# Kernel tuning notes

Measured on AMD Instinct MI355X. Metric: run time of the kernel, lower is better.

The kernel has to match this reference:

```python
import jax, jax.numpy as jnp
import numpy as np

EPS = 1e-8

def setup_inputs() -> dict:
    key = jax.random.key(0)
    k1, k2 = jax.random.split(key)
    B, IN, OUT, G = 32768, 256, 256, 5
    x = jax.random.normal(k1, (B, IN), dtype=jnp.float32)
    grid = jnp.linspace(-1.0, 1.0, G).astype(jnp.float32)
    coef = jax.random.normal(k2, (OUT, IN, G), dtype=jnp.float32) * 0.1
    scale = jnp.ones((OUT, IN), dtype=jnp.float32)
    bias = jnp.zeros((OUT,), dtype=jnp.float32)
    return {"x": x, "grid": grid, "coef": coef, "scale": scale, "bias": bias}

def reference(x, grid, coef, scale, bias):
    # global min-max normalization to [-1, 1]
    xmin, xmax = x.min(), x.max()
    xn = 2.0 * (x - xmin) / (xmax - xmin + EPS) - 1.0
    # cubic bump B-spline-like basis: (batch, in, grid)
    dist = jnp.abs(xn[..., None] - grid)
    basis = jnp.where(dist < 1.0, 1.0 - dist ** 3, 0.0)
    basis = basis / (basis.sum(axis=-1, keepdims=True) + EPS)
    # fused contraction over (in, grid); equals ((basis*coef).sum(-1)*scale).sum(-1)
    w = coef * scale[..., None]          # (out, in, grid)
    out = jnp.einsum('big,oig->bo', basis, w) + bias
    return out
```

## Files before the change

### kernel.cpp

```cpp
#include <hip/hip_runtime.h>
#include <stdint.h>


#define B_SZ   32768
#define IN_SZ  256
#define OUT_SZ 256
#define EPSF   1e-8f
#define NMB    2048

typedef __bf16 bf16x8 __attribute__((ext_vector_type(8)));
typedef unsigned short ushort8 __attribute__((ext_vector_type(8)));
typedef float floatx4 __attribute__((ext_vector_type(4)));

union frag_u { uint4 u; bf16x8 v; };

__device__ __forceinline__ unsigned short f2bf(float f) {
  unsigned u = __float_as_uint(f);
  u += 0x7FFFu + ((u >> 16) & 1u);
  return (unsigned short)(u >> 16);
}


__global__ void __launch_bounds__(256) prep_kernel(const float* __restrict__ coef,
                                                   const float* __restrict__ scale,
                                                   const float* __restrict__ x,
                                                   unsigned short* __restrict__ wf,
                                                   float* __restrict__ part, int n4) {
  const int t = threadIdx.x;
  if (blockIdx.x < 256) {
    int idx = blockIdx.x * 256 + t;
    int o = idx >> 8, i = idx & 255;
    float s = scale[idx];
    const float* c = coef + (size_t)idx * 5;
    ushort8 v;
    v[0] = f2bf(c[0] * s); v[1] = f2bf(c[1] * s); v[2] = f2bf(c[2] * s);
    v[3] = f2bf(c[3] * s); v[4] = f2bf(c[4] * s);
    v[5] = 0; v[6] = 0; v[7] = 0;
    int cb = o >> 4, om = o & 15;
    *(ushort8*)(wf + ((size_t)((cb * 256 + i) * 16 + om)) * 8) = v;
  } else {
    int mb = blockIdx.x - 256;
    const float4* x4 = (const float4*)x;
    int i = mb * 256 + t;
    float lmin = 1e30f, lmax = -1e30f;
    #pragma unroll
    for (int k = 0; k < 4; ++k) {
      float4 v = x4[i + k * (NMB * 256)];
      lmin = fminf(lmin, fminf(fminf(v.x, v.y), fminf(v.z, v.w)));
      lmax = fmaxf(lmax, fmaxf(fmaxf(v.x, v.y), fmaxf(v.z, v.w)));
    }
    #pragma unroll
    for (int off = 32; off >= 1; off >>= 1) {
      lmin = fminf(lmin, __shfl_down(lmin, off, 64));
      lmax = fmaxf(lmax, __shfl_down(lmax, off, 64));
    }
    __shared__ float smn[4], smx[4];
    if ((t & 63) == 0) { smn[t >> 6] = lmin; smx[t >> 6] = lmax; }
    __syncthreads();
    if (t == 0) {
      part[2 * mb]     = fminf(fminf(smn[0], smn[1]), fminf(smn[2], smn[3]));
      part[2 * mb + 1] = fmaxf(fmaxf(smx[0], smx[1]), fmaxf(smx[2], smx[3]));
    }
  }
}

__device__ __forceinline__ bf16x8 basisfrag(float xval, float scA, float scB) {
  float xn = fmaf(xval, scA, scB);
  float d0 = xn + 1.0f, d1 = xn + 0.5f, d3 = xn - 0.5f, d4 = xn - 1.0f;
  float b0 = fmaxf(fmaf(d0 * d0, -fabsf(d0), 1.0f), 0.0f);
  float b1 = fmaxf(fmaf(d1 * d1, -fabsf(d1), 1.0f), 0.0f);
  float b2 = fmaxf(fmaf(xn * xn, -fabsf(xn), 1.0f), 0.0f);
  float b3 = fmaxf(fmaf(d3 * d3, -fabsf(d3), 1.0f), 0.0f);
  float b4 = fmaxf(fmaf(d4 * d4, -fabsf(d4), 1.0f), 0.0f);
  float sum = ((b0 + b1) + (b2 + b3)) + b4;
  float inv = __builtin_amdgcn_rcpf(sum);
  b0 *= inv; b1 *= inv; b2 *= inv; b3 *= inv; b4 *= inv;
  frag_u r;
  r.u.x = __builtin_amdgcn_perm(__float_as_uint(b1), __float_as_uint(b0), 0x07060302u);
  r.u.y = __builtin_amdgcn_perm(__float_as_uint(b3), __float_as_uint(b2), 0x07060302u);
  r.u.z = __float_as_uint(b4) >> 16;
  r.u.w = 0u;
  return r.v;
}

__global__ void __launch_bounds__(256, 4) kan_gemm(
    const float* __restrict__ x,
    const unsigned short* __restrict__ wf,
    const float* __restrict__ bias,
    const float* __restrict__ part,
    float* __restrict__ out)
{
  __shared__ __align__(16) unsigned short Bb[2][8192];
  __shared__ float2 red[4];

  const int t = threadIdx.x;
  const int lane = t & 63;
  const int wm = t >> 6;
  const int l15 = lane & 15, koff = lane >> 4;
  const int bRow = blockIdx.x * 64;
  const int bCol = blockIdx.y * 128;
  const int row = bRow + wm * 16 + l15;

  auto stage = [&](int c, int buf) {
    #pragma unroll
    for (int r = 0; r < 4; ++r) {
      int s = r * 4 + wm;
      int cb = blockIdx.y * 8 + (s & 7);
      int i0 = c * 8 + (s >> 3) * 4;
      const unsigned short* src = wf + ((size_t)(cb * 256 + i0) * 16) * 8
                                     + (size_t)lane * 8;
      __builtin_amdgcn_global_load_lds(
          (const __attribute__((address_space(1))) unsigned int*)src,
          (__attribute__((address_space(3))) unsigned int*)(&Bb[buf][s * 512 + lane * 8]),
          16, 0, 0);
    }
  };

  const float* xrow = x + (size_t)row * IN_SZ;

  float xc0 = xrow[koff];
  float xc1 = xrow[4 + koff];
  stage(0, 0);

  float mn = 1e30f, mx = -1e30f;
  const float2* part2 = (const float2*)part;
  #pragma unroll
  for (int k = 0; k < NMB / 256; ++k) {
    float2 p = part2[k * 256 + t];
    mn = fminf(mn, p.x); mx = fmaxf(mx, p.y);
  }
  #pragma unroll
  for (int off = 32; off >= 1; off >>= 1) {
    mn = fminf(mn, __shfl_down(mn, off, 64));
    mx = fmaxf(mx, __shfl_down(mx, off, 64));
  }
  if (lane == 0) red[wm] = make_float2(mn, mx);
  __syncthreads();
  mn = fminf(fminf(red[0].x, red[1].x), fminf(red[2].x, red[3].x));
  mx = fmaxf(fmaxf(red[0].y, red[1].y), fmaxf(red[2].y, red[3].y));
  const float scA = 2.0f / (mx - mn + EPSF);
  const float scB = -mn * scA - 1.0f;

  floatx4 acc[8] = {};
  bf16x8 bf[8];

  auto ldsB = [&](int ktr, int buf) {
    #pragma unroll
    for (int q = 0; q < 8; ++q)
      bf[q] = *(const bf16x8*)(&Bb[buf][(ktr * 8 + q) * 512 + lane * 8]);
  };

  for (int c = 0; c < 32; ++c) {
    const int buf = c & 1;
    float xn0, xn1;

    if (c < 31) {
      xn0 = xrow[(c + 1) * 8 + koff];
      xn1 = xrow[(c + 1) * 8 + 4 + koff];
      stage(c + 1, buf ^ 1);
    }
    __builtin_amdgcn_sched_barrier(0);
    if (c < 31) asm volatile("s_waitcnt vmcnt(6)");
    else        asm volatile("s_waitcnt vmcnt(0)");
    __builtin_amdgcn_s_barrier();
    __builtin_amdgcn_sched_barrier(0);

    ldsB(0, buf);
    {
      bf16x8 a = basisfrag(xc0, scA, scB);
      __builtin_amdgcn_s_setprio(1);
      #pragma unroll
      for (int q = 0; q < 8; ++q)
        acc[q] = __builtin_amdgcn_mfma_f32_16x16x32_bf16(a, bf[q], acc[q], 0, 0, 0);
      __builtin_amdgcn_s_setprio(0);
    }
    ldsB(1, buf);
    {
      bf16x8 a = basisfrag(xc1, scA, scB);
      __builtin_amdgcn_s_setprio(1);
      #pragma unroll
      for (int q = 0; q < 8; ++q)
        acc[q] = __builtin_amdgcn_mfma_f32_16x16x32_bf16(a, bf[q], acc[q], 0, 0, 0);
      __builtin_amdgcn_s_setprio(0);
    }

    if (c < 31) {
      xc0 = xn0; xc1 = xn1;
      __builtin_amdgcn_sched_barrier(0);
      __builtin_amdgcn_s_barrier();
      __builtin_amdgcn_sched_barrier(0);
    }
  }

  #pragma unroll
  for (int q = 0; q < 8; ++q) {
    int o = bCol + q * 16 + l15;
    float bs = bias[o];
    int rb = bRow + wm * 16 + koff * 4;
    #pragma unroll
    for (int reg = 0; reg < 4; ++reg)
      out[(size_t)(rb + reg) * OUT_SZ + o] = acc[q][reg] + bs;
  }
}

extern "C" void kernel_launch(void* const* d_in, const int* in_sizes, int n_in,
                              void* d_out, int out_size, void* d_ws, size_t ws_size,
                              hipStream_t stream) {
  const float* x     = (const float*)d_in[0];
  const float* coef  = (const float*)d_in[2];
  const float* scale = (const float*)d_in[3];
  const float* bias  = (const float*)d_in[4];
  float* out = (float*)d_out;

  size_t need = 16384 + (size_t)OUT_SZ * IN_SZ * 8 * 2;
  if (ws_size < need) return;

  float* part = (float*)d_ws;
  unsigned short* wf = (unsigned short*)((char*)d_ws + 16384);

  prep_kernel<<<256 + NMB, 256, 0, stream>>>(coef, scale, x, wf, part,
                                             (B_SZ * IN_SZ) / 4);
  dim3 g(B_SZ / 64, OUT_SZ / 128);
  kan_gemm<<<g, 256, 0, stream>>>(x, wf, bias, part, out);
}
```

Measured before the change: 143.4 us.

## Switch to 32x32x16 MFMA with split-K across waves and LDS reduction

Replaces the 16x16x32 bf16 MFMA tiling with 32x32x16 MFMAs. Each wave now covers a 32-row slab and half of the input dimension (split-K over two wave pairs), and the two partial accumulators are reduced through LDS in the epilogue. The weight layout in the prep kernel and the staging addresses are reshuffled to match the new fragment layout, and x is loaded as float4. This is meant to raise MFMA throughput per instruction and cut basis computation per wave, at the cost of an extra LDS reduction pass and a changed waitcnt.

```diff
diff --git a/kernel.cpp b/kernel.cpp
--- a/kernel.cpp
+++ b/kernel.cpp
@@ -10,7 +10,7 @@
 
 typedef __bf16 bf16x8 __attribute__((ext_vector_type(8)));
 typedef unsigned short ushort8 __attribute__((ext_vector_type(8)));
-typedef float floatx4 __attribute__((ext_vector_type(4)));
+typedef float floatx16 __attribute__((ext_vector_type(16)));
 
 union frag_u { uint4 u; bf16x8 v; };
 
@@ -36,8 +36,9 @@
     v[0] = f2bf(c[0] * s); v[1] = f2bf(c[1] * s); v[2] = f2bf(c[2] * s);
     v[3] = f2bf(c[3] * s); v[4] = f2bf(c[4] * s);
     v[5] = 0; v[6] = 0; v[7] = 0;
-    int cb = o >> 4, om = o & 15;
-    *(ushort8*)(wf + ((size_t)((cb * 256 + i) * 16 + om)) * 8) = v;
+    int chunk = (((o >> 5) * 64 + (i >> 2)) * 2 + ((i >> 1) & 1)) * 64
+                + (i & 1) * 32 + (o & 31);
+    *(ushort8*)(wf + (size_t)chunk * 8) = v;
   } else {
     int mb = blockIdx.x - 256;
     const float4* x4 = (const float4*)x;
@@ -96,30 +97,31 @@
   const int t = threadIdx.x;
   const int lane = t & 63;
   const int wm = t >> 6;
-  const int l15 = lane & 15, koff = lane >> 4;
+  const int sm = wm & 1;
+  const int h  = wm >> 1;
+  const int l31 = lane & 31, lh = lane >> 5;
   const int bRow = blockIdx.x * 64;
   const int bCol = blockIdx.y * 128;
-  const int row = bRow + wm * 16 + l15;
+  const int row = bRow + sm * 32 + l31;
 
   auto stage = [&](int c, int buf) {
     #pragma unroll
     for (int r = 0; r < 4; ++r) {
-      int s = r * 4 + wm;
-      int cb = blockIdx.y * 8 + (s & 7);
-      int i0 = c * 8 + (s >> 3) * 4;
-      const unsigned short* src = wf + ((size_t)(cb * 256 + i0) * 16) * 8
-                                     + (size_t)lane * 8;
+      int seg = r * 4 + wm;
+      int sh = seg >> 3, sks = (seg >> 2) & 1, sot = seg & 3;
+      const unsigned short* src = wf +
+          ((size_t)(((blockIdx.y * 4 + sot) * 64 + (sh * 32 + c)) * 2 + sks)) * 512
+          + (size_t)lane * 8;
       __builtin_amdgcn_global_load_lds(
           (const __attribute__((address_space(1))) unsigned int*)src,
-          (__attribute__((address_space(3))) unsigned int*)(&Bb[buf][s * 512 + lane * 8]),
+          (__attribute__((address_space(3))) unsigned int*)(&Bb[buf][seg * 512 + lane * 8]),
           16, 0, 0);
     }
   };
 
-  const float* xrow = x + (size_t)row * IN_SZ;
-
-  float xc0 = xrow[koff];
-  float xc1 = xrow[4 + koff];
+  const float* xrow = x + (size_t)row * IN_SZ + h * 128;
+
+  float4 xq = *(const float4*)(xrow);
   stage(0, 0);
 
   float mn = 1e30f, mx = -1e30f;
@@ -141,65 +143,80 @@
   const float scA = 2.0f / (mx - mn + EPSF);
   const float scB = -mn * scA - 1.0f;
 
-  floatx4 acc[8] = {};
+  floatx16 acc[4] = {};
   bf16x8 bf[8];
-
-  auto ldsB = [&](int ktr, int buf) {
-    #pragma unroll
-    for (int q = 0; q < 8; ++q)
-      bf[q] = *(const bf16x8*)(&Bb[buf][(ktr * 8 + q) * 512 + lane * 8]);
-  };
 
   for (int c = 0; c < 32; ++c) {
     const int buf = c & 1;
-    float xn0, xn1;
+    float4 xn;
 
     if (c < 31) {
-      xn0 = xrow[(c + 1) * 8 + koff];
-      xn1 = xrow[(c + 1) * 8 + 4 + koff];
+      xn = *(const float4*)(xrow + (c + 1) * 4);
       stage(c + 1, buf ^ 1);
     }
     __builtin_amdgcn_sched_barrier(0);
-    if (c < 31) asm volatile("s_waitcnt vmcnt(6)");
+    if (c < 31) asm volatile("s_waitcnt vmcnt(5)");
     else        asm volatile("s_waitcnt vmcnt(0)");
     __builtin_amdgcn_s_barrier();
     __builtin_amdgcn_sched_barrier(0);
 
-    ldsB(0, buf);
-    {
-      bf16x8 a = basisfrag(xc0, scA, scB);
-      __builtin_amdgcn_s_setprio(1);
-      #pragma unroll
-      for (int q = 0; q < 8; ++q)
-        acc[q] = __builtin_amdgcn_mfma_f32_16x16x32_bf16(a, bf[q], acc[q], 0, 0, 0);
-      __builtin_amdgcn_s_setprio(0);
-    }
-    ldsB(1, buf);
-    {
-      bf16x8 a = basisfrag(xc1, scA, scB);
-      __builtin_amdgcn_s_setprio(1);
-      #pragma unroll
-      for (int q = 0; q < 8; ++q)
-        acc[q] = __builtin_amdgcn_mfma_f32_16x16x32_bf16(a, bf[q], acc[q], 0, 0, 0);
-      __builtin_amdgcn_s_setprio(0);
-    }
+    #pragma unroll
+    for (int q = 0; q < 8; ++q) {
+      int ni = q >> 1, ks = q & 1;
+      bf[q] = *(const bf16x8*)(&Bb[buf][(h * 8 + ks * 4 + ni) * 512 + lane * 8]);
+    }
+
+    float xv0 = lh ? xq.y : xq.x;
+    float xv1 = lh ? xq.w : xq.z;
+    bf16x8 a0 = basisfrag(xv0, scA, scB);
+    bf16x8 a1 = basisfrag(xv1, scA, scB);
+
+    __builtin_amdgcn_s_setprio(1);
+    #pragma unroll
+    for (int ni = 0; ni < 4; ++ni) {
+      acc[ni] = __builtin_amdgcn_mfma_f32_32x32x16_bf16(a0, bf[ni * 2 + 0], acc[ni], 0, 0, 0);
+      acc[ni] = __builtin_amdgcn_mfma_f32_32x32x16_bf16(a1, bf[ni * 2 + 1], acc[ni], 0, 0, 0);
+    }
+    __builtin_amdgcn_s_setprio(0);
 
     if (c < 31) {
-      xc0 = xn0; xc1 = xn1;
+      xq = xn;
       __builtin_amdgcn_sched_barrier(0);
       __builtin_amdgcn_s_barrier();
       __builtin_amdgcn_sched_barrier(0);
     }
   }
 
-  #pragma unroll
-  for (int q = 0; q < 8; ++q) {
-    int o = bCol + q * 16 + l15;
-    float bs = bias[o];
-    int rb = bRow + wm * 16 + koff * 4;
-    #pragma unroll
-    for (int reg = 0; reg < 4; ++reg)
-      out[(size_t)(rb + reg) * OUT_SZ + o] = acc[q][reg] + bs;
+  __syncthreads();
+  float* Cb = (float*)Bb;
+  {
+    int eo = h ? 0 : 2;
+    int e  = h ? 0 : 1;
+    float* base = Cb + (sm * 2 + e) * 2048;
+    #pragma unroll
+    for (int ni2 = 0; ni2 < 2; ++ni2) {
+      #pragma unroll
+      for (int reg = 0; reg < 16; ++reg) {
+        int r = 4 * lh + (reg & 3) + 8 * (reg >> 2);
+        base[r * 64 + ni2 * 32 + l31] = acc[eo + ni2][reg];
+      }
+    }
+  }
+  __syncthreads();
+  {
+    int ko = h ? 2 : 0;
+    const float* base = Cb + (sm * 2 + h) * 2048;
+    #pragma unroll
+    for (int ni2 = 0; ni2 < 2; ++ni2) {
+      int o = bCol + h * 64 + ni2 * 32 + l31;
+      float bs = bias[o];
+      #pragma unroll
+      for (int reg = 0; reg < 16; ++reg) {
+        int r = 4 * lh + (reg & 3) + 8 * (reg >> 2);
+        float v = acc[ko + ni2][reg] + base[r * 64 + ni2 * 32 + l31] + bs;
+        out[(size_t)(bRow + sm * 32 + r) * OUT_SZ + o] = v;
+      }
+    }
   }
 }
 
```

Result: faster. 140.4 us (-2.1%).
